# Kernel optimization log

Hardware: AMD Instinct MI355X
Metric: run time of the kernel (lower is better)

## Reference

```python
import jax, jax.numpy as jnp
import numpy as np

DIM = 1024
SEGMENT_SIZE = 1024
DILATION_RATE = 2

def setup_inputs() -> dict:
    key = jax.random.key(0)
    x = jax.random.normal(key, (4, 8192, DIM), dtype=jnp.float32)
    return {"x": x}

def reference(x) -> jnp.ndarray:
    B, S, D = x.shape
    pad = (-S) % SEGMENT_SIZE
    x = jnp.pad(x, ((0, 0), (0, pad), (0, 0)))
    # [B, n_seg, segment_size, D]
    x = x.reshape(B, -1, SEGMENT_SIZE, D)
    # dilation: strided slice within each segment -> [B, n_seg, seg', D]
    x = x[:, :, ::DILATION_RATE, :]
    q = k = v = x
    scale = 1.0 / jnp.sqrt(jnp.asarray(D, dtype=x.dtype))
    # attention within each segment over dilated tokens (non-causal, no dropout)
    scores = jnp.einsum('bsqd,bskd->bsqk', q, k) * scale
    probs = jax.nn.softmax(scores, axis=-1)
    attn = jnp.einsum('bsqk,bskd->bsqd', probs, v)
    # flatten segments back to a (shortened, dilated) sequence
    return attn.reshape(B, -1, D)
```

## Files before the change

### kernel.cpp

```cpp
#include <hip/hip_runtime.h>


typedef float          f32x4  __attribute__((ext_vector_type(4)));
typedef short          bf16x8 __attribute__((ext_vector_type(8)));

#define MFMA16(a, b, c) __builtin_amdgcn_mfma_f32_16x16x32_bf16((a), (b), (c), 0, 0, 0)

static __device__ __forceinline__ unsigned short f2bf(float f) {
    unsigned u = __float_as_uint(f);
    u = (u + 0x7fffu + ((u >> 16) & 1u)) >> 16;
    return (unsigned short)u;
}

static __device__ __forceinline__ void async_cp16(const unsigned short* g, unsigned short* l) {
    __builtin_amdgcn_global_load_lds((const __attribute__((address_space(1))) unsigned int*)g,
                                     (__attribute__((address_space(3))) unsigned int*)l,
                                     16, 0, 0);
}

static __device__ __forceinline__ void stage_tile(const unsigned short* __restrict__ src,
                                                  unsigned short* lds,
                                                  int row_stride, int col0,
                                                  int wave, int lane) {
    const int pr = lane >> 3;
    const int lc = (lane & 7) ^ pr;
    #pragma unroll
    for (int c = 0; c < 4; ++c) {
        const int chunk = wave * 4 + c;
        async_cp16(src + (size_t)(chunk * 8 + pr) * row_stride + col0 + lc * 8,
                   lds + chunk * 512);
    }
}

__global__ __launch_bounds__(256) void k_prep(const float* __restrict__ x,
                                              unsigned short* __restrict__ Xb,
                                              unsigned short* __restrict__ VT,
                                              float* __restrict__ Lsum) {
    const int kb = blockIdx.x, db = blockIdx.y, g = blockIdx.z;
    const int t = threadIdx.x;
    if (kb == 0 && db == 0) {
        Lsum[g * 512 + t] = 0.f;
        Lsum[g * 512 + 256 + t] = 0.f;
    }
    __shared__ unsigned short Ts[64][72];
    {
        const int r = t >> 2, q = t & 3;
        const float* src = x + ((size_t)g << 20) + (size_t)(kb * 64 + r) * 2048 + db * 64 + q * 16;
        alignas(16) unsigned short tmp[16];
        #pragma unroll
        for (int i = 0; i < 4; ++i) {
            const float4 v = *reinterpret_cast<const float4*>(src + i * 4);
            tmp[i * 4 + 0] = f2bf(v.x); tmp[i * 4 + 1] = f2bf(v.y);
            tmp[i * 4 + 2] = f2bf(v.z); tmp[i * 4 + 3] = f2bf(v.w);
        }
        unsigned short* xb = Xb + ((size_t)g * 512 + kb * 64 + r) * 1024 + db * 64 + q * 16;
        *reinterpret_cast<uint4*>(xb)     = *reinterpret_cast<const uint4*>(&tmp[0]);
        *reinterpret_cast<uint4*>(xb + 8) = *reinterpret_cast<const uint4*>(&tmp[8]);
        *reinterpret_cast<uint4*>(&Ts[r][q * 16])     = *reinterpret_cast<const uint4*>(&tmp[0]);
        *reinterpret_cast<uint4*>(&Ts[r][q * 16 + 8]) = *reinterpret_cast<const uint4*>(&tmp[8]);
    }
    __syncthreads();
    {
        const int dl = t >> 2, kq = t & 3;
        alignas(16) unsigned short o[16];
        #pragma unroll
        for (int j = 0; j < 16; ++j) o[j] = Ts[kq * 16 + j][dl];
        unsigned short* vt = VT + ((size_t)g * 1024 + db * 64 + dl) * 512 + kb * 64 + kq * 16;
        *reinterpret_cast<uint4*>(vt)     = *reinterpret_cast<const uint4*>(&o[0]);
        *reinterpret_cast<uint4*>(vt + 8) = *reinterpret_cast<const uint4*>(&o[8]);
    }
}

__global__ __launch_bounds__(256) void k_scores(const unsigned short* __restrict__ Xb,
                                                unsigned short* __restrict__ T,
                                                float* __restrict__ Lsum) {
    const int g = blockIdx.x, item = blockIdx.y;
    const int mb = (item < 4) ? 0 : (item < 7) ? 1 : (item < 9) ? 2 : 3;
    const int start = (mb == 0) ? 0 : (mb == 1) ? 4 : (mb == 2) ? 7 : 9;
    const int nb = mb + (item - start);
    const bool diag = (mb == nb);

    const int tid = threadIdx.x, wave = tid >> 6, lane = tid & 63;
    const int g4 = lane >> 4, n16 = lane & 15;
    const int wr = wave & 1, wc = wave >> 1;

    __shared__ unsigned short As[128 * 64];
    __shared__ unsigned short Bs[128 * 64];
    __shared__ float red[4][64];

    const unsigned short* Ag = Xb + ((size_t)g * 512 + mb * 128) * 1024;
    const unsigned short* Bg = Xb + ((size_t)g * 512 + nb * 128) * 1024;

    f32x4 acc[16];
    const f32x4 vzero = {0.f, 0.f, 0.f, 0.f};
    #pragma unroll
    for (int i = 0; i < 16; ++i) acc[i] = vzero;

    for (int kt = 0; kt < 16; ++kt) {
        if (kt) __syncthreads();
        stage_tile(Ag, As, 1024, kt * 64, wave, lane);
        stage_tile(Bg, Bs, 1024, kt * 64, wave, lane);
        __syncthreads();
        #pragma unroll
        for (int ks = 0; ks < 2; ++ks) {
            const int sw = ((ks * 4 + g4) ^ (n16 & 7)) * 8;
            bf16x8 a[4], b[4];
            #pragma unroll
            for (int i = 0; i < 4; ++i)
                a[i] = *reinterpret_cast<const bf16x8*>(&As[(wr * 64 + i * 16 + n16) * 64 + sw]);
            #pragma unroll
            for (int j = 0; j < 4; ++j)
                b[j] = *reinterpret_cast<const bf16x8*>(&Bs[(wc * 64 + j * 16 + n16) * 64 + sw]);
            #pragma unroll
            for (int i = 0; i < 4; ++i)
                #pragma unroll
                for (int j = 0; j < 4; ++j)
                    acc[i * 4 + j] = MFMA16(a[i], b[j], acc[i * 4 + j]);
        }
    }

    float rs[4][4];
    float cs[4];
    #pragma unroll
    for (int i = 0; i < 4; ++i)
        #pragma unroll
        for (int r = 0; r < 4; ++r) rs[i][r] = 0.f;
    #pragma unroll
    for (int j = 0; j < 4; ++j) cs[j] = 0.f;

    unsigned short* Tg = T + ((size_t)g * 512 + mb * 128 + wr * 64) * 512 + nb * 128 + wc * 64;
    unsigned short* Tm = T + ((size_t)g * 512 + nb * 128 + wc * 64) * 512 + mb * 128 + wr * 64;
    #pragma unroll
    for (int i = 0; i < 4; ++i)
        #pragma unroll
        for (int j = 0; j < 4; ++j) {
            unsigned pk[2];
            #pragma unroll
            for (int r = 0; r < 4; ++r) {
                const float e = __expf(acc[i * 4 + j][r] * 0.03125f);
                rs[i][r] += e;
                cs[j] += e;
                const unsigned short h = f2bf(e);
                Tg[(size_t)(i * 16 + g4 * 4 + r) * 512 + j * 16 + n16] = h;
                if (r & 1) pk[r >> 1] |= (unsigned)h << 16;
                else       pk[r >> 1]  = h;
            }
            if (!diag) {
                *reinterpret_cast<uint2*>(
                    &Tm[(size_t)(j * 16 + n16) * 512 + i * 16 + g4 * 4]) =
                    make_uint2(pk[0], pk[1]);
            }
        }

    #pragma unroll
    for (int d = 1; d < 16; d <<= 1)
        #pragma unroll
        for (int i = 0; i < 4; ++i)
            #pragma unroll
            for (int r = 0; r < 4; ++r)
                rs[i][r] += __shfl_xor(rs[i][r], d, 64);
    if (n16 == 0) {
        #pragma unroll
        for (int i = 0; i < 4; ++i)
            #pragma unroll
            for (int r = 0; r < 4; ++r)
                red[wave][i * 16 + g4 * 4 + r] = rs[i][r];
    }

    if (!diag) {
        #pragma unroll
        for (int j = 0; j < 4; ++j) {
            float c = cs[j];
            c += __shfl_xor(c, 16, 64);
            c += __shfl_xor(c, 32, 64);
            if (g4 == 0)
                atomicAdd(&Lsum[g * 512 + nb * 128 + wc * 64 + j * 16 + n16], c);
        }
    }

    __syncthreads();
    if (tid < 128) {
        const int h = tid >> 6, idx = tid & 63;
        atomicAdd(&Lsum[g * 512 + mb * 128 + h * 64 + idx],
                  red[h][idx] + red[h + 2][idx]);
    }
}

__global__ __launch_bounds__(256) void k_pv(const unsigned short* __restrict__ T,
                                            const unsigned short* __restrict__ VT,
                                            const float* __restrict__ Lsum,
                                            float* __restrict__ out) {
    const int g = blockIdx.x, nb = blockIdx.y, mb = blockIdx.z;
    const int tid = threadIdx.x, wave = tid >> 6, lane = tid & 63;
    const int g4 = lane >> 4, n16 = lane & 15;
    const int wr = wave & 1, wc = wave >> 1;

    __shared__ unsigned short As[128 * 64];
    __shared__ unsigned short Bs[128 * 64];
    __shared__ float Linv[128];

    if (tid < 128) Linv[tid] = 1.0f / Lsum[g * 512 + mb * 128 + tid];

    const unsigned short* Ag = T  + ((size_t)g * 512  + mb * 128) * 512;
    const unsigned short* Bg = VT + ((size_t)g * 1024 + nb * 128) * 512;

    f32x4 acc[16];
    const f32x4 vzero = {0.f, 0.f, 0.f, 0.f};
    #pragma unroll
    for (int i = 0; i < 16; ++i) acc[i] = vzero;

    for (int kt = 0; kt < 8; ++kt) {
        __syncthreads();
        stage_tile(Ag, As, 512, kt * 64, wave, lane);
        stage_tile(Bg, Bs, 512, kt * 64, wave, lane);
        __syncthreads();
        #pragma unroll
        for (int ks = 0; ks < 2; ++ks) {
            const int sw = ((ks * 4 + g4) ^ (n16 & 7)) * 8;
            bf16x8 a[4], b[4];
            #pragma unroll
            for (int i = 0; i < 4; ++i)
                a[i] = *reinterpret_cast<const bf16x8*>(&As[(wr * 64 + i * 16 + n16) * 64 + sw]);
            #pragma unroll
            for (int j = 0; j < 4; ++j)
                b[j] = *reinterpret_cast<const bf16x8*>(&Bs[(wc * 64 + j * 16 + n16) * 64 + sw]);
            #pragma unroll
            for (int i = 0; i < 4; ++i)
                #pragma unroll
                for (int j = 0; j < 4; ++j)
                    acc[i * 4 + j] = MFMA16(a[i], b[j], acc[i * 4 + j]);
        }
    }

    float li[4][4];
    #pragma unroll
    for (int i = 0; i < 4; ++i)
        #pragma unroll
        for (int r = 0; r < 4; ++r)
            li[i][r] = Linv[wr * 64 + i * 16 + g4 * 4 + r];

    float* og = out + ((size_t)g * 512 + mb * 128 + wr * 64) * 1024 + nb * 128 + wc * 64;
    #pragma unroll
    for (int i = 0; i < 4; ++i)
        #pragma unroll
        for (int j = 0; j < 4; ++j)
            #pragma unroll
            for (int r = 0; r < 4; ++r)
                og[(size_t)(i * 16 + g4 * 4 + r) * 1024 + j * 16 + n16] =
                    acc[i * 4 + j][r] * li[i][r];
}

extern "C" void kernel_launch(void* const* d_in, const int* in_sizes, int n_in,
                              void* d_out, int out_size, void* d_ws, size_t ws_size,
                              hipStream_t stream) {
    const float* x = (const float*)d_in[0];
    float* out = (float*)d_out;

    unsigned short* T  = (unsigned short*)d_ws;
    unsigned short* Xb = T  + (size_t)32 * 512 * 512;
    unsigned short* VT = Xb + (size_t)32 * 512 * 1024;
    float*          Ls = (float*)(VT + (size_t)32 * 1024 * 512);

    k_prep  <<<dim3(8, 16, 32), 256, 0, stream>>>(x, Xb, VT, Ls);
    k_scores<<<dim3(32, 10),    256, 0, stream>>>(Xb, T, Ls);
    k_pv    <<<dim3(32, 8, 4),  256, 0, stream>>>(T, VT, Ls, out);
}
```

Before: 246.7 us.

## Load MFMA operands directly from global memory, dropping LDS staging in GEMM kernels

The scores and PV GEMM kernels now read bf16 operand fragments straight from global memory into registers instead of staging 128x64 tiles through LDS with async copies and two barriers per k-step. This removes the LDS traffic and block synchronisation, and lets more blocks fit per CU, with a launch-bounds occupancy hint of 3. The cost is redundant global or L2 reads, since each wave re-fetches rows that other waves also need, and partially coalesced 16-byte loads. The prep kernel's transpose tile also gets an XOR swizzle to reduce LDS bank conflicts.

```diff
diff --git a/kernel.cpp b/kernel.cpp
--- a/kernel.cpp
+++ b/kernel.cpp
@@ -10,26 +10,6 @@
     unsigned u = __float_as_uint(f);
     u = (u + 0x7fffu + ((u >> 16) & 1u)) >> 16;
     return (unsigned short)u;
-}
-
-static __device__ __forceinline__ void async_cp16(const unsigned short* g, unsigned short* l) {
-    __builtin_amdgcn_global_load_lds((const __attribute__((address_space(1))) unsigned int*)g,
-                                     (__attribute__((address_space(3))) unsigned int*)l,
-                                     16, 0, 0);
-}
-
-static __device__ __forceinline__ void stage_tile(const unsigned short* __restrict__ src,
-                                                  unsigned short* lds,
-                                                  int row_stride, int col0,
-                                                  int wave, int lane) {
-    const int pr = lane >> 3;
-    const int lc = (lane & 7) ^ pr;
-    #pragma unroll
-    for (int c = 0; c < 4; ++c) {
-        const int chunk = wave * 4 + c;
-        async_cp16(src + (size_t)(chunk * 8 + pr) * row_stride + col0 + lc * 8,
-                   lds + chunk * 512);
-    }
 }
 
 __global__ __launch_bounds__(256) void k_prep(const float* __restrict__ x,
@@ -56,24 +36,27 @@
         unsigned short* xb = Xb + ((size_t)g * 512 + kb * 64 + r) * 1024 + db * 64 + q * 16;
         *reinterpret_cast<uint4*>(xb)     = *reinterpret_cast<const uint4*>(&tmp[0]);
         *reinterpret_cast<uint4*>(xb + 8) = *reinterpret_cast<const uint4*>(&tmp[8]);
-        *reinterpret_cast<uint4*>(&Ts[r][q * 16])     = *reinterpret_cast<const uint4*>(&tmp[0]);
-        *reinterpret_cast<uint4*>(&Ts[r][q * 16 + 8]) = *reinterpret_cast<const uint4*>(&tmp[8]);
+        const int r4 = r >> 4;
+        const int cA = (2 * q) ^ r4, cB = (2 * q + 1) ^ r4;
+        *reinterpret_cast<uint4*>(&Ts[r][cA * 8]) = *reinterpret_cast<const uint4*>(&tmp[0]);
+        *reinterpret_cast<uint4*>(&Ts[r][cB * 8]) = *reinterpret_cast<const uint4*>(&tmp[8]);
     }
     __syncthreads();
     {
         const int dl = t >> 2, kq = t & 3;
         alignas(16) unsigned short o[16];
         #pragma unroll
-        for (int j = 0; j < 16; ++j) o[j] = Ts[kq * 16 + j][dl];
+        for (int j = 0; j < 16; ++j)
+            o[j] = Ts[kq * 16 + j][(((dl >> 3) ^ kq) << 3) | (dl & 7)];
         unsigned short* vt = VT + ((size_t)g * 1024 + db * 64 + dl) * 512 + kb * 64 + kq * 16;
         *reinterpret_cast<uint4*>(vt)     = *reinterpret_cast<const uint4*>(&o[0]);
         *reinterpret_cast<uint4*>(vt + 8) = *reinterpret_cast<const uint4*>(&o[8]);
     }
 }
 
-__global__ __launch_bounds__(256) void k_scores(const unsigned short* __restrict__ Xb,
-                                                unsigned short* __restrict__ T,
-                                                float* __restrict__ Lsum) {
+__global__ __launch_bounds__(256, 3) void k_scores(const unsigned short* __restrict__ Xb,
+                                                   unsigned short* __restrict__ T,
+                                                   float* __restrict__ Lsum) {
     const int g = blockIdx.x, item = blockIdx.y;
     const int mb = (item < 4) ? 0 : (item < 7) ? 1 : (item < 9) ? 2 : 3;
     const int start = (mb == 0) ? 0 : (mb == 1) ? 4 : (mb == 2) ? 7 : 9;
@@ -84,33 +67,35 @@
     const int g4 = lane >> 4, n16 = lane & 15;
     const int wr = wave & 1, wc = wave >> 1;
 
-    __shared__ unsigned short As[128 * 64];
-    __shared__ unsigned short Bs[128 * 64];
     __shared__ float red[4][64];
 
-    const unsigned short* Ag = Xb + ((size_t)g * 512 + mb * 128) * 1024;
-    const unsigned short* Bg = Xb + ((size_t)g * 512 + nb * 128) * 1024;
+    const unsigned short* Ar[4];
+    const unsigned short* Br[4];
+    #pragma unroll
+    for (int i = 0; i < 4; ++i)
+        Ar[i] = Xb + ((size_t)g * 512 + mb * 128 + wr * 64 + i * 16 + n16) * 1024;
+    #pragma unroll
+    for (int j = 0; j < 4; ++j)
+        Br[j] = Xb + ((size_t)g * 512 + nb * 128 + wc * 64 + j * 16 + n16) * 1024;
 
     f32x4 acc[16];
     const f32x4 vzero = {0.f, 0.f, 0.f, 0.f};
     #pragma unroll
     for (int i = 0; i < 16; ++i) acc[i] = vzero;
 
+    #pragma unroll 1
     for (int kt = 0; kt < 16; ++kt) {
-        if (kt) __syncthreads();
-        stage_tile(Ag, As, 1024, kt * 64, wave, lane);
-        stage_tile(Bg, Bs, 1024, kt * 64, wave, lane);
-        __syncthreads();
+        const int k0 = kt * 64;
         #pragma unroll
         for (int ks = 0; ks < 2; ++ks) {
-            const int sw = ((ks * 4 + g4) ^ (n16 & 7)) * 8;
+            const int ko = k0 + (ks * 4 + g4) * 8;
             bf16x8 a[4], b[4];
             #pragma unroll
             for (int i = 0; i < 4; ++i)
-                a[i] = *reinterpret_cast<const bf16x8*>(&As[(wr * 64 + i * 16 + n16) * 64 + sw]);
+                a[i] = *reinterpret_cast<const bf16x8*>(Ar[i] + ko);
             #pragma unroll
             for (int j = 0; j < 4; ++j)
-                b[j] = *reinterpret_cast<const bf16x8*>(&Bs[(wc * 64 + j * 16 + n16) * 64 + sw]);
+                b[j] = *reinterpret_cast<const bf16x8*>(Br[j] + ko);
             #pragma unroll
             for (int i = 0; i < 4; ++i)
                 #pragma unroll
@@ -186,44 +171,45 @@
     }
 }
 
-__global__ __launch_bounds__(256) void k_pv(const unsigned short* __restrict__ T,
-                                            const unsigned short* __restrict__ VT,
-                                            const float* __restrict__ Lsum,
-                                            float* __restrict__ out) {
+__global__ __launch_bounds__(256, 3) void k_pv(const unsigned short* __restrict__ T,
+                                               const unsigned short* __restrict__ VT,
+                                               const float* __restrict__ Lsum,
+                                               float* __restrict__ out) {
     const int g = blockIdx.x, nb = blockIdx.y, mb = blockIdx.z;
     const int tid = threadIdx.x, wave = tid >> 6, lane = tid & 63;
     const int g4 = lane >> 4, n16 = lane & 15;
     const int wr = wave & 1, wc = wave >> 1;
 
-    __shared__ unsigned short As[128 * 64];
-    __shared__ unsigned short Bs[128 * 64];
     __shared__ float Linv[128];
-
     if (tid < 128) Linv[tid] = 1.0f / Lsum[g * 512 + mb * 128 + tid];
 
-    const unsigned short* Ag = T  + ((size_t)g * 512  + mb * 128) * 512;
-    const unsigned short* Bg = VT + ((size_t)g * 1024 + nb * 128) * 512;
+    const unsigned short* Ar[4];
+    const unsigned short* Br[4];
+    #pragma unroll
+    for (int i = 0; i < 4; ++i)
+        Ar[i] = T  + ((size_t)g * 512  + mb * 128 + wr * 64 + i * 16 + n16) * 512;
+    #pragma unroll
+    for (int j = 0; j < 4; ++j)
+        Br[j] = VT + ((size_t)g * 1024 + nb * 128 + wc * 64 + j * 16 + n16) * 512;
 
     f32x4 acc[16];
     const f32x4 vzero = {0.f, 0.f, 0.f, 0.f};
     #pragma unroll
     for (int i = 0; i < 16; ++i) acc[i] = vzero;
 
+    #pragma unroll 1
     for (int kt = 0; kt < 8; ++kt) {
-        __syncthreads();
-        stage_tile(Ag, As, 512, kt * 64, wave, lane);
-        stage_tile(Bg, Bs, 512, kt * 64, wave, lane);
-        __syncthreads();
+        const int k0 = kt * 64;
         #pragma unroll
         for (int ks = 0; ks < 2; ++ks) {
-            const int sw = ((ks * 4 + g4) ^ (n16 & 7)) * 8;
+            const int ko = k0 + (ks * 4 + g4) * 8;
             bf16x8 a[4], b[4];
             #pragma unroll
             for (int i = 0; i < 4; ++i)
-                a[i] = *reinterpret_cast<const bf16x8*>(&As[(wr * 64 + i * 16 + n16) * 64 + sw]);
+                a[i] = *reinterpret_cast<const bf16x8*>(Ar[i] + ko);
             #pragma unroll
             for (int j = 0; j < 4; ++j)
-                b[j] = *reinterpret_cast<const bf16x8*>(&Bs[(wc * 64 + j * 16 + n16) * 64 + sw]);
+                b[j] = *reinterpret_cast<const bf16x8*>(Br[j] + ko);
             #pragma unroll
             for (int i = 0; i < 4; ++i)
                 #pragma unroll
@@ -231,6 +217,7 @@
                     acc[i * 4 + j] = MFMA16(a[i], b[j], acc[i * 4 + j]);
         }
     }
+    __syncthreads();
 
     float li[4][4];
     #pragma unroll
```

Measured after the change: 321.1 us. +30.2%, slower.
